# Kernel optimization log

Measured on AMD Instinct MI355X. Metric: run time of the kernel, lower is better.

The kernel has to match this reference:

```python
import jax, jax.numpy as jnp
import numpy as np

D = 256; NH = 8; NL = 4; NP = 4; DFF = 2048; HD = D // NH
SHAPES = [(64, 64), (32, 32), (16, 16), (8, 8)]
B = 2; LEN = sum(h * w for h, w in SHAPES)


def setup_inputs() -> dict:
    key = jax.random.key(0)
    ks = jax.random.split(key, 12)
    def w(k, shape, s=0.02):
        return jax.random.normal(k, shape, jnp.float32) * s
    starts = np.cumsum([0] + [h * w for h, w in SHAPES[:-1]])
    return {
        "src": jax.random.normal(ks[0], (B, LEN, D), jnp.float32),
        "pos": jax.random.normal(ks[1], (B, LEN, D), jnp.float32) * 0.1,
        "spatial_shapes": jnp.array(SHAPES, dtype=jnp.int32),
        "level_start_index": jnp.array(starts, dtype=jnp.int32),
        "w_value": w(ks[2], (D, D)), "b_value": jnp.zeros((D,), jnp.float32),
        "w_off": w(ks[3], (D, NH * NL * NP * 2)), "b_off": w(ks[4], (NH * NL * NP * 2,), 0.1),
        "w_attn": w(ks[5], (D, NH * NL * NP)), "b_attn": jnp.zeros((NH * NL * NP,), jnp.float32),
        "w_out": w(ks[6], (D, D)), "b_out": jnp.zeros((D,), jnp.float32),
        "w1": w(ks[7], (D, DFF)), "b1": jnp.zeros((DFF,), jnp.float32),
        "w2": w(ks[8], (DFF, D)), "b2": jnp.zeros((D,), jnp.float32),
        "g1": jnp.ones((D,), jnp.float32), "be1": jnp.zeros((D,), jnp.float32),
        "g2": jnp.ones((D,), jnp.float32), "be2": jnp.zeros((D,), jnp.float32),
    }


def _layer_norm(x, g, b):
    mu = jnp.mean(x, -1, keepdims=True)
    v = jnp.var(x, -1, keepdims=True)
    return (x - mu) * jax.lax.rsqrt(v + 1e-5) * g + b


def _reference_points(shapes):
    # torch.linspace(0.5, H-0.5, H)/H == (arange(H)+0.5)/H
    refs = []
    for H, W in shapes:
        ry = (jnp.arange(H, dtype=jnp.float32) + 0.5) / H
        rx = (jnp.arange(W, dtype=jnp.float32) + 0.5) / W
        yy, xx = jnp.meshgrid(ry, rx, indexing='ij')
        refs.append(jnp.stack([xx.ravel(), yy.ravel()], -1))
    return jnp.concatenate(refs, 0)  # (Len, 2) as (x, y)


def _ms_deform_sample(value, loc, shapes):
    # value: (B, Len, NH, HD); loc: (B, Lq, NH, NL, NP, 2) normalized [0,1]
    # Replicates torch grid_sample(bilinear, padding='zeros', align_corners=False).
    Bn, Lq = loc.shape[0], loc.shape[1]
    P = loc.shape[4]
    start = 0
    outs = []
    for lvl, (H, W) in enumerate(shapes):
        v = value[:, start:start + H * W].transpose(0, 2, 1, 3)  # (B, NH, HW, HD)
        start += H * W
        l = loc[:, :, :, lvl]                      # (B, Lq, NH, P, 2)
        x = l[..., 0] * W - 0.5
        y = l[..., 1] * H - 0.5
        x0 = jnp.floor(x); y0 = jnp.floor(y)
        dx = x - x0; dy = y - y0
        x0i = x0.astype(jnp.int32); y0i = y0.astype(jnp.int32)
        acc = None
        for xi, yi, wgt in ((x0i, y0i, (1 - dx) * (1 - dy)),
                            (x0i + 1, y0i, dx * (1 - dy)),
                            (x0i, y0i + 1, (1 - dx) * dy),
                            (x0i + 1, y0i + 1, dx * dy)):
            valid = ((xi >= 0) & (xi < W) & (yi >= 0) & (yi < H)).astype(value.dtype)
            idx = jnp.clip(yi, 0, H - 1) * W + jnp.clip(xi, 0, W - 1)  # (B, Lq, NH, P)
            idx = idx.transpose(0, 2, 1, 3).reshape(Bn, NH, Lq * P)
            g = jnp.take_along_axis(v, idx[..., None], axis=2).reshape(Bn, NH, Lq, P, HD)
            w = (wgt * valid).transpose(0, 2, 1, 3)[..., None]  # (B, NH, Lq, P, 1)
            acc = g * w if acc is None else acc + g * w
        outs.append(acc)  # (B, NH, Lq, P, HD)
    return jnp.stack(outs, 3)  # (B, NH, Lq, NL, NP, HD)


def _forward(src, pos, w_value, b_value, w_off, b_off, w_attn, b_attn,
             w_out, b_out, w1, b1, w2, b2, g1, be1, g2, be2, shapes):
    Bn, Lq, _ = src.shape
    q = src + pos  # with_pos_embed
    value = (src @ w_value + b_value).reshape(Bn, Lq, NH, HD)
    off = (q @ w_off + b_off).reshape(Bn, Lq, NH, NL, NP, 2)
    attn = jax.nn.softmax((q @ w_attn + b_attn).reshape(Bn, Lq, NH, NL * NP), -1)
    attn = attn.reshape(Bn, Lq, NH, NL, NP)
    ref = _reference_points(shapes)  # (Len, 2)
    normalizer = jnp.array([[w_, h_] for h_, w_ in shapes], jnp.float32)  # (NL, 2) = (W, H)
    loc = ref[None, :, None, None, None, :] + off / normalizer[None, None, None, :, None, :]
    sampled = _ms_deform_sample(value, loc, shapes)  # (B, NH, Lq, NL, NP, HD)
    out = jnp.einsum('bqhlp,bhqlpd->bqhd', attn, sampled).reshape(Bn, Lq, D)
    out = out @ w_out + b_out
    x = _layer_norm(src + out, g1, be1)           # residual + norm1
    ff = jax.nn.relu(x @ w1 + b1) @ w2 + b2       # FFN (dropout=0)
    return _layer_norm(x + ff, g2, be2)           # residual + norm2


def reference(src, pos, spatial_shapes, level_start_index, w_value, b_value,
              w_off, b_off, w_attn, b_attn, w_out, b_out, w1, b1, w2, b2,
              g1, be1, g2, be2):
    shapes = [tuple(int(v) for v in s) for s in np.asarray(spatial_shapes)]
    return _forward(src, pos, w_value, b_value, w_off, b_off, w_attn, b_attn,
                    w_out, b_out, w1, b1, w2, b2, g1, be1, g2, be2, shapes)
```

## Files before the change

kernel.cpp:

```cpp
#include <hip/hip_runtime.h>
#include <math.h>

#define D 256
#define NH 8
#define NL 4
#define NP 4
#define DFF 2048
#define HD 32
#define BB 2
#define LEN 5440
#define MROWS (BB * LEN)

typedef __attribute__((ext_vector_type(8))) short short8;
typedef __attribute__((ext_vector_type(4))) float f32x4;
typedef unsigned int uint32;

__device__ __forceinline__ unsigned short f2bf(float f) {
    uint32 u = __float_as_uint(f);
    u += 0x7FFF + ((u >> 16) & 1);
    return (unsigned short)(u >> 16);
}
__device__ __forceinline__ float bf2f(unsigned short h) {
    return __uint_as_float(((uint32)h) << 16);
}
__device__ __forceinline__ uint32 pack2(float a, float b) {
    return (uint32)f2bf(a) | ((uint32)f2bf(b) << 16);
}

__device__ __forceinline__ void gl16(const unsigned short* g, unsigned short* l) {
    __builtin_amdgcn_global_load_lds(
        (const __attribute__((address_space(1))) unsigned int*)g,
        (__attribute__((address_space(3))) unsigned int*)l, 16, 0, 0);
}

__device__ __forceinline__ void swz85(int b, int ncols, int& row, int& col) {
    const int gsz = ncols << 3;
    const int full = 10 * gsz;
    if (b < full) {
        const int g = b / gsz, idx = b - g * gsz;
        row = (g << 3) + (idx & 7);
        col = idx >> 3;
    } else {
        const int idx = b - full;
        row = 80 + idx % 5;
        col = idx / 5;
    }
}

__global__ void prep(const float* __restrict__ w_value, const float* __restrict__ w_off,
                     const float* __restrict__ w_attn, const float* __restrict__ w_out,
                     const float* __restrict__ w1, const float* __restrict__ w2,
                     const float* __restrict__ b_value, const float* __restrict__ b_off,
                     const float* __restrict__ b_attn,
                     unsigned short* __restrict__ wqvT, unsigned short* __restrict__ woT,
                     unsigned short* __restrict__ w1T, unsigned short* __restrict__ w2T,
                     float* __restrict__ bqv) {
    const int blk = blockIdx.x;
    if (blk >= 1248) {
        for (int i = threadIdx.x; i < 640; i += 256)
            bqv[i] = (i < 256) ? b_value[i] : (i < 512 ? b_off[i - 256] : b_attn[i - 512]);
        return;
    }
    const float* W; unsigned short* WT; int K, N, tid;
    if (blk < 64)       { W = w_value; WT = wqvT;             K = 256;  N = 256;  tid = blk; }
    else if (blk < 128) { W = w_off;   WT = wqvT + 256 * 256; K = 256;  N = 256;  tid = blk - 64; }
    else if (blk < 160) { W = w_attn;  WT = wqvT + 512 * 256; K = 256;  N = 128;  tid = blk - 128; }
    else if (blk < 224) { W = w_out;   WT = woT;              K = 256;  N = 256;  tid = blk - 160; }
    else if (blk < 736) { W = w1;      WT = w1T;              K = 256;  N = 2048; tid = blk - 224; }
    else                { W = w2;      WT = w2T;              K = 2048; N = 256;  tid = blk - 736; }
    const int ntx = N >> 5;
    const int nb = (tid % ntx) * 32, kb = (tid / ntx) * 32;

    __shared__ float tile[32][33];
    const int tx = threadIdx.x & 31, ty = threadIdx.x >> 5;
#pragma unroll
    for (int i = 0; i < 32; i += 8)
        tile[ty + i][tx] = W[(size_t)(kb + ty + i) * N + nb + tx];
    __syncthreads();
#pragma unroll
    for (int i = 0; i < 32; i += 8)
        WT[(size_t)(nb + ty + i) * K + kb + tx] = f2bf(tile[tx][ty + i]);
}

__global__ __launch_bounds__(256) void ffn1_gemm(
        const unsigned short* __restrict__ A,
        const unsigned short* __restrict__ BT, const float* __restrict__ bias,
        unsigned short* __restrict__ Cv, int N, int K, int lda, int ldb) {
    __shared__ unsigned short Ash[2][128][32];
    __shared__ unsigned short Bsh[2][128][32];

    int rowt, colt;
    swz85(blockIdx.x, N >> 7, rowt, colt);
    const int row0 = rowt * 128, col0 = colt * 128;

    const int t = threadIdx.x;
    const int wave = t >> 6, lane = t & 63;
    const int wr = wave >> 1, wc = wave & 1;
    const int lrow = lane & 15, quad = lane >> 4;
    const int sr = lane >> 2, sc = (lane & 3) * 8;

    const unsigned short* Ab = A + (size_t)row0 * lda;
    const unsigned short* Bb = BT + (size_t)col0 * ldb;

    f32x4 acc[4][4];
#pragma unroll
    for (int i = 0; i < 4; i++)
#pragma unroll
        for (int j = 0; j < 4; j++) acc[i][j] = (f32x4){0.f, 0.f, 0.f, 0.f};

    auto stage = [&](int buf, int kb) {
#pragma unroll
        for (int j = 0; j < 2; j++) {
            const int r = wave * 32 + j * 16;
            gl16(Ab + (size_t)(r + sr) * lda + kb + sc, &Ash[buf][r][0]);
            gl16(Bb + (size_t)(r + sr) * ldb + kb + sc, &Bsh[buf][r][0]);
        }
    };

    stage(0, 0);
    int i = 0;
    for (int kb = 0; kb < K; kb += 32, ++i) {
        __syncthreads();
        if (kb + 32 < K) stage((i + 1) & 1, kb + 32);
        const int cf = i & 1;
        short8 af[4], bfr[4];
#pragma unroll
        for (int mt = 0; mt < 4; mt++)
            af[mt] = *(const short8*)&Ash[cf][wr * 64 + mt * 16 + lrow][quad * 8];
#pragma unroll
        for (int nt = 0; nt < 4; nt++)
            bfr[nt] = *(const short8*)&Bsh[cf][wc * 64 + nt * 16 + lrow][quad * 8];
#pragma unroll
        for (int mt = 0; mt < 4; mt++)
#pragma unroll
            for (int nt = 0; nt < 4; nt++)
                acc[mt][nt] = __builtin_amdgcn_mfma_f32_16x16x32_bf16(
                    af[mt], bfr[nt], acc[mt][nt], 0, 0, 0);
    }

#pragma unroll
    for (int nt = 0; nt < 4; nt++) {
        const int col = col0 + wc * 64 + nt * 16 + lrow;
        const float bv = bias[col];
#pragma unroll
        for (int mt = 0; mt < 4; mt++) {
            f32x4 a = acc[mt][nt];
#pragma unroll
            for (int r = 0; r < 4; r++) {
                const int row = row0 + wr * 64 + mt * 16 + quad * 4 + r;
                Cv[(size_t)row * N + col] = f2bf(fmaxf(a[r] + bv, 0.f));
            }
        }
    }
}

template <int NZ>
__global__ __launch_bounds__(256) void splitk_gemm(
        const unsigned short* __restrict__ A, const unsigned short* __restrict__ BT,
        unsigned short* __restrict__ part, int KC, int lda, int ldb) {
    __shared__ unsigned short Ash[2][128][32];
    __shared__ unsigned short Bsh[2][128][32];

    int rowt, cc;
    swz85(blockIdx.x, 2 * NZ, rowt, cc);
    const int row0 = rowt * 128;
    const int col0 = (cc & 1) * 128;
    const int z = cc >> 1;
    const int koff = z * KC;
    unsigned short* __restrict__ C = part + (size_t)z * MROWS * 256;

    const int t = threadIdx.x;
    const int wave = t >> 6, lane = t & 63;
    const int wr = wave >> 1, wc = wave & 1;
    const int lrow = lane & 15, quad = lane >> 4;
    const int sr = lane >> 2, sc = (lane & 3) * 8;

    const unsigned short* Ab = A + (size_t)row0 * lda + koff;
    const unsigned short* Bb = BT + (size_t)col0 * ldb + koff;

    f32x4 acc[4][4];
#pragma unroll
    for (int i = 0; i < 4; i++)
#pragma unroll
        for (int j = 0; j < 4; j++) acc[i][j] = (f32x4){0.f, 0.f, 0.f, 0.f};

    auto stage = [&](int buf, int kb) {
#pragma unroll
        for (int j = 0; j < 2; j++) {
            const int r = wave * 32 + j * 16;
            gl16(Ab + (size_t)(r + sr) * lda + kb + sc, &Ash[buf][r][0]);
            gl16(Bb + (size_t)(r + sr) * ldb + kb + sc, &Bsh[buf][r][0]);
        }
    };

    stage(0, 0);
    int i = 0;
    for (int kb = 0; kb < KC; kb += 32, ++i) {
        __syncthreads();
        if (kb + 32 < KC) stage((i + 1) & 1, kb + 32);
        const int cf = i & 1;
        short8 af[4], bfr[4];
#pragma unroll
        for (int mt = 0; mt < 4; mt++)
            af[mt] = *(const short8*)&Ash[cf][wr * 64 + mt * 16 + lrow][quad * 8];
#pragma unroll
        for (int nt = 0; nt < 4; nt++)
            bfr[nt] = *(const short8*)&Bsh[cf][wc * 64 + nt * 16 + lrow][quad * 8];
#pragma unroll
        for (int mt = 0; mt < 4; mt++)
#pragma unroll
            for (int nt = 0; nt < 4; nt++)
                acc[mt][nt] = __builtin_amdgcn_mfma_f32_16x16x32_bf16(
                    af[mt], bfr[nt], acc[mt][nt], 0, 0, 0);
    }

#pragma unroll
    for (int nt = 0; nt < 4; nt++) {
        const int col = col0 + wc * 64 + nt * 16 + lrow;
#pragma unroll
        for (int mt = 0; mt < 4; mt++) {
            f32x4 a = acc[mt][nt];
#pragma unroll
            for (int r = 0; r < 4; r++) {
                const int row = row0 + wr * 64 + mt * 16 + quad * 4 + r;
                C[(size_t)row * 256 + col] = f2bf(a[r]);
            }
        }
    }
}

__global__ __launch_bounds__(256) void gemm_ln(
        const unsigned short* __restrict__ A, const unsigned short* __restrict__ BT,
        const float* __restrict__ bias, const float* __restrict__ rsd,
        const float* __restrict__ g, const float* __restrict__ be,
        unsigned short* __restrict__ out16, int K) {
    __shared__ unsigned short Ash[2][32][32];
    __shared__ unsigned short Bsh[2][256][32];
    __shared__ float red1[4][32], red2[4][32];

    const int row0 = blockIdx.x * 32;
    const int t = threadIdx.x;
    const int wave = t >> 6, lane = t & 63;
    const int lrow = lane & 15, quad = lane >> 4;
    const int sr = lane >> 2, sc = (lane & 3) * 8;

    f32x4 acc[2][4];
#pragma unroll
    for (int i = 0; i < 2; i++)
#pragma unroll
        for (int j = 0; j < 4; j++) acc[i][j] = (f32x4){0.f, 0.f, 0.f, 0.f};

    auto stage = [&](int buf, int kb) {
#pragma unroll
        for (int j = 0; j < 4; j++) {
            const int r = wave * 64 + j * 16;
            gl16(BT + (size_t)(r + sr) * K + kb + sc, &Bsh[buf][r][0]);
        }
        if (wave < 2) {
            const int r = wave * 16;
            gl16(A + (size_t)(row0 + r + sr) * K + kb + sc, &Ash[buf][r][0]);
        }
    };

    stage(0, 0);
    int it = 0;
    for (int kb = 0; kb < K; kb += 32, ++it) {
        __syncthreads();
        if (kb + 32 < K) stage((it + 1) & 1, kb + 32);
        const int cf = it & 1;
        short8 af[2], bfr[4];
#pragma unroll
        for (int mt = 0; mt < 2; mt++)
            af[mt] = *(const short8*)&Ash[cf][mt * 16 + lrow][quad * 8];
#pragma unroll
        for (int nt = 0; nt < 4; nt++)
            bfr[nt] = *(const short8*)&Bsh[cf][wave * 64 + nt * 16 + lrow][quad * 8];
#pragma unroll
        for (int mt = 0; mt < 2; mt++)
#pragma unroll
            for (int nt = 0; nt < 4; nt++)
                acc[mt][nt] = __builtin_amdgcn_mfma_f32_16x16x32_bf16(
                    af[mt], bfr[nt], acc[mt][nt], 0, 0, 0);
    }

    float gv[4], bev[4], bv[4];
#pragma unroll
    for (int nt = 0; nt < 4; nt++) {
        const int col = wave * 64 + nt * 16 + lrow;
        bv[nt] = bias[col];
        gv[nt] = g[col];
        bev[nt] = be[col];
    }

    float v[2][4][4];
#pragma unroll
    for (int mt = 0; mt < 2; mt++)
#pragma unroll
        for (int r = 0; r < 4; r++) {
            const int row = row0 + mt * 16 + quad * 4 + r;
#pragma unroll
            for (int nt = 0; nt < 4; nt++) {
                const int col = wave * 64 + nt * 16 + lrow;
                v[mt][nt][r] = acc[mt][nt][r] + bv[nt] + rsd[(size_t)row * 256 + col];
            }
        }

#pragma unroll
    for (int mt = 0; mt < 2; mt++)
#pragma unroll
        for (int r = 0; r < 4; r++) {
            float s1 = v[mt][0][r] + v[mt][1][r] + v[mt][2][r] + v[mt][3][r];
            float s2 = v[mt][0][r] * v[mt][0][r] + v[mt][1][r] * v[mt][1][r] +
                       v[mt][2][r] * v[mt][2][r] + v[mt][3][r] * v[mt][3][r];
#pragma unroll
            for (int o = 1; o < 16; o <<= 1) {
                s1 += __shfl_xor(s1, o, 16);
                s2 += __shfl_xor(s2, o, 16);
            }
            if (lrow == 0) {
                const int rr = mt * 16 + quad * 4 + r;
                red1[wave][rr] = s1;
                red2[wave][rr] = s2;
            }
        }
    __syncthreads();

#pragma unroll
    for (int mt = 0; mt < 2; mt++)
#pragma unroll
        for (int r = 0; r < 4; r++) {
            const int rr = mt * 16 + quad * 4 + r;
            const float su = red1[0][rr] + red1[1][rr] + red1[2][rr] + red1[3][rr];
            const float sq = red2[0][rr] + red2[1][rr] + red2[2][rr] + red2[3][rr];
            const float mean = su * (1.0f / 256.0f);
            const float var = fmaxf(sq * (1.0f / 256.0f) - mean * mean, 0.f);
            const float rstd = rsqrtf(var + 1e-5f);
            const size_t rowoff = (size_t)(row0 + rr) * 256;
#pragma unroll
            for (int nt = 0; nt < 4; nt++) {
                const int col = wave * 64 + nt * 16 + lrow;
                const float o = (v[mt][nt][r] - mean) * rstd * gv[nt] + bev[nt];
                out16[rowoff + col] = f2bf(o);
            }
        }
}

__global__ __launch_bounds__(256) void qv_gemm(
        const float* __restrict__ src, const float* __restrict__ pos,
        const unsigned short* __restrict__ BT, const float* __restrict__ bias,
        unsigned short* __restrict__ val, unsigned short* __restrict__ qout16) {
    __shared__ unsigned short Ash[2][128][40];
    __shared__ unsigned short Bsh[2][128][32];

    int rowt, colt;
    swz85(blockIdx.x, 5, rowt, colt);
    const int row0 = rowt * 128, col0 = colt * 128;
    const bool addp = (col0 >= 256);

    const int t = threadIdx.x;
    const int wave = t >> 6, lane = t & 63;
    const int wr = wave >> 1, wc = wave & 1;
    const int lrow = lane & 15, quad = lane >> 4;
    const int srow = t >> 1;
    const int cb = (t & 1) * 16;
    const int sr = lane >> 2, sc = (lane & 3) * 8;

    const float* ap = src + (size_t)(row0 + srow) * 256 + cb;
    const float* pp = pos + (size_t)(row0 + srow) * 256 + cb;
    const unsigned short* Bb = BT + (size_t)col0 * 256;

    f32x4 acc[4][4];
#pragma unroll
    for (int i = 0; i < 4; i++)
#pragma unroll
        for (int j = 0; j < 4; j++) acc[i][j] = (f32x4){0.f, 0.f, 0.f, 0.f};

    float4 fa[4]; float4 fp[4];
    auto packA = [&](int buf) {
        float4 f0 = fa[0], f1 = fa[1], f2 = fa[2], f3 = fa[3];
        if (addp) {
            f0.x += fp[0].x; f0.y += fp[0].y; f0.z += fp[0].z; f0.w += fp[0].w;
            f1.x += fp[1].x; f1.y += fp[1].y; f1.z += fp[1].z; f1.w += fp[1].w;
            f2.x += fp[2].x; f2.y += fp[2].y; f2.z += fp[2].z; f2.w += fp[2].w;
            f3.x += fp[3].x; f3.y += fp[3].y; f3.z += fp[3].z; f3.w += fp[3].w;
        }
        uint4 u0 = make_uint4(pack2(f0.x, f0.y), pack2(f0.z, f0.w),
                              pack2(f1.x, f1.y), pack2(f1.z, f1.w));
        uint4 u1 = make_uint4(pack2(f2.x, f2.y), pack2(f2.z, f2.w),
                              pack2(f3.x, f3.y), pack2(f3.z, f3.w));
        *(uint4*)&Ash[buf][srow][cb + 0] = u0;
        *(uint4*)&Ash[buf][srow][cb + 8] = u1;
    };
    auto loadA = [&](int kb) {
#pragma unroll
        for (int j = 0; j < 4; j++) fa[j] = *(const float4*)(ap + kb + 4 * j);
        if (addp) {
#pragma unroll
            for (int j = 0; j < 4; j++) fp[j] = *(const float4*)(pp + kb + 4 * j);
        }
    };
    auto stageB = [&](int buf, int kb) {
#pragma unroll
        for (int j = 0; j < 2; j++) {
            const int r = wave * 32 + j * 16;
            gl16(Bb + (size_t)(r + sr) * 256 + kb + sc, &Bsh[buf][r][0]);
        }
    };

    loadA(0);
    packA(0);
    stageB(0, 0);
    loadA(32);

    int i = 0;
    for (int kb = 0; kb < 256; kb += 32, ++i) {
        __syncthreads();
        if (kb + 32 < 256) {
            stageB((i + 1) & 1, kb + 32);
            packA((i + 1) & 1);
            if (kb + 64 < 256) loadA(kb + 64);
        }
        const int cf = i & 1;
        short8 af[4], bfr[4];
#pragma unroll
        for (int mt = 0; mt < 4; mt++)
            af[mt] = *(const short8*)&Ash[cf][wr * 64 + mt * 16 + lrow][quad * 8];
#pragma unroll
        for (int nt = 0; nt < 4; nt++)
            bfr[nt] = *(const short8*)&Bsh[cf][wc * 64 + nt * 16 + lrow][quad * 8];
#pragma unroll
        for (int mt = 0; mt < 4; mt++)
#pragma unroll
            for (int nt = 0; nt < 4; nt++)
                acc[mt][nt] = __builtin_amdgcn_mfma_f32_16x16x32_bf16(
                    af[mt], bfr[nt], acc[mt][nt], 0, 0, 0);
    }

#pragma unroll
    for (int nt = 0; nt < 4; nt++) {
        const int col = col0 + wc * 64 + nt * 16 + lrow;
        const float bv = bias[col];
#pragma unroll
        for (int mt = 0; mt < 4; mt++) {
            f32x4 a = acc[mt][nt];
#pragma unroll
            for (int r = 0; r < 4; r++) {
                const int row = row0 + wr * 64 + mt * 16 + quad * 4 + r;
                float v = a[r] + bv;
                if (col < 256)
                    val[(size_t)row * 256 + col] = f2bf(v);
                else
                    qout16[(size_t)row * 384 + (col - 256)] = f2bf(v);
            }
        }
    }
}

__global__ void sampler(const unsigned short* __restrict__ val,
                        const unsigned short* __restrict__ qout16,
                        unsigned short* __restrict__ out) {
    __shared__ __align__(16) int   sIdx[2][128][4];
    __shared__ __align__(16) float sW[2][128][4];
    const int t = threadIdx.x;
    const int sub = t >> 7;
    const int tt = t & 127;
    const int bq = blockIdx.x * 2 + sub;
    const int b = bq / LEN, q = bq % LEN;

    {
        const int h = tt >> 4, p = tt & 15;
        const int l = p >> 2;

        float refx, refy;
        if (q < 4096) {
            int rq = q >> 6, cq = q & 63;
            refx = (cq + 0.5f) * (1.0f / 64.0f);
            refy = (rq + 0.5f) * (1.0f / 64.0f);
        } else if (q < 5120) {
            int qq = q - 4096;
            int rq = qq >> 5, cq = qq & 31;
            refx = (cq + 0.5f) * (1.0f / 32.0f);
            refy = (rq + 0.5f) * (1.0f / 32.0f);
        } else if (q < 5376) {
            int qq = q - 5120;
            int rq = qq >> 4, cq = qq & 15;
            refx = (cq + 0.5f) * (1.0f / 16.0f);
            refy = (rq + 0.5f) * (1.0f / 16.0f);
        } else {
            int qq = q - 5376;
            int rq = qq >> 3, cq = qq & 7;
            refx = (cq + 0.5f) * (1.0f / 8.0f);
            refy = (rq + 0.5f) * (1.0f / 8.0f);
        }

        float lv = bf2f(qout16[(size_t)bq * 384 + 256 + tt]);
        float mx = lv;
#pragma unroll
        for (int o = 1; o < 16; o <<= 1) mx = fmaxf(mx, __shfl_xor(mx, o, 16));
        float e = expf(lv - mx);
        float s = e;
#pragma unroll
        for (int o = 1; o < 16; o <<= 1) s += __shfl_xor(s, o, 16);
        const float aw = e / s;

        const uint32 opair = *(const uint32*)&qout16[(size_t)bq * 384 + h * 32 + p * 2];
        const float ox = bf2f((unsigned short)opair);
        const float oy = bf2f((unsigned short)(opair >> 16));

        const int LST[4] = {0, 4096, 5120, 5376};
        const int WW = 64 >> l;
        const float rw = 1.0f / (float)WW;

        float x = (refx + ox * rw) * (float)WW - 0.5f;
        float y = (refy + oy * rw) * (float)WW - 0.5f;
        float x0f = floorf(x), y0f = floorf(y);
        float dx = x - x0f, dy = y - y0f;
        int x0 = (int)x0f, y0 = (int)y0f;

        const int base = (b * LEN + LST[l]) * 256 + h * 32;
        int xs[2] = {x0, x0 + 1}, ys[2] = {y0, y0 + 1};
        float wx[2] = {1.f - dx, dx}, wy[2] = {1.f - dy, dy};
        int ic[4]; float wc4[4];
#pragma unroll
        for (int cy = 0; cy < 2; cy++)
#pragma unroll
            for (int cx = 0; cx < 2; cx++) {
                int xi = xs[cx], yi = ys[cy];
                bool vld = (xi >= 0) && (xi < WW) && (yi >= 0) && (yi < WW);
                int xc = min(max(xi, 0), WW - 1);
                int yc = min(max(yi, 0), WW - 1);
                ic[cy * 2 + cx] = base + (yc * WW + xc) * 256;
                wc4[cy * 2 + cx] = vld ? wx[cx] * wy[cy] * aw : 0.f;
            }
        *(int4*)&sIdx[sub][tt][0] = make_int4(ic[0], ic[1], ic[2], ic[3]);
        *(float4*)&sW[sub][tt][0] = make_float4(wc4[0], wc4[1], wc4[2], wc4[3]);
    }
    __syncthreads();

    const int h = tt >> 4, dp = tt & 15;
    const unsigned short* vald = val + 2 * dp;
    float acc0 = 0.f, acc1 = 0.f;
#pragma unroll 4
    for (int p = 0; p < 16; p++) {
        const int r = h * 16 + p;
        int4 iv = *(const int4*)&sIdx[sub][r][0];
        float4 wv = *(const float4*)&sW[sub][r][0];
        uint32 u0 = *(const uint32*)(vald + iv.x);
        uint32 u1 = *(const uint32*)(vald + iv.y);
        uint32 u2 = *(const uint32*)(vald + iv.z);
        uint32 u3 = *(const uint32*)(vald + iv.w);
        acc0 += bf2f((unsigned short)u0) * wv.x + bf2f((unsigned short)u1) * wv.y +
                bf2f((unsigned short)u2) * wv.z + bf2f((unsigned short)u3) * wv.w;
        acc1 += bf2f((unsigned short)(u0 >> 16)) * wv.x + bf2f((unsigned short)(u1 >> 16)) * wv.y +
                bf2f((unsigned short)(u2 >> 16)) * wv.z + bf2f((unsigned short)(u3 >> 16)) * wv.w;
    }
    *(uint32*)&out[(size_t)bq * D + h * HD + 2 * dp] = pack2(acc0, acc1);
}

__global__ void add_ln4(const unsigned short* __restrict__ part16,
                        const float* __restrict__ bias,
                        const unsigned short* __restrict__ rsd16,
                        const float* __restrict__ g, const float* __restrict__ be,
                        float* __restrict__ out) {
    const int wave = threadIdx.x >> 6, lane = threadIdx.x & 63;
    const int row = blockIdx.x * 4 + wave;
    const int c0 = lane * 4;
    const size_t i = (size_t)row * 256 + c0;

    float v[4];
    {
        ushort4 r = *(const ushort4*)&rsd16[i];
        float4 bv = *(const float4*)&bias[c0];
        v[0] = bf2f(r.x) + bv.x; v[1] = bf2f(r.y) + bv.y;
        v[2] = bf2f(r.z) + bv.z; v[3] = bf2f(r.w) + bv.w;
    }
#pragma unroll
    for (int z = 0; z < 4; z++) {
        ushort4 p = *(const ushort4*)&part16[(size_t)z * MROWS * 256 + i];
        v[0] += bf2f(p.x); v[1] += bf2f(p.y); v[2] += bf2f(p.z); v[3] += bf2f(p.w);
    }
    float s1 = v[0] + v[1] + v[2] + v[3];
    float s2 = v[0] * v[0] + v[1] * v[1] + v[2] * v[2] + v[3] * v[3];
#pragma unroll
    for (int o = 32; o > 0; o >>= 1) {
        s1 += __shfl_xor(s1, o, 64);
        s2 += __shfl_xor(s2, o, 64);
    }
    const float mean = s1 * (1.0f / 256.0f);
    const float var = fmaxf(s2 * (1.0f / 256.0f) - mean * mean, 0.f);
    const float rstd = rsqrtf(var + 1e-5f);

    float4 gv = *(const float4*)&g[c0];
    float4 bev = *(const float4*)&be[c0];
    float4 o4;
    o4.x = (v[0] - mean) * rstd * gv.x + bev.x;
    o4.y = (v[1] - mean) * rstd * gv.y + bev.y;
    o4.z = (v[2] - mean) * rstd * gv.z + bev.z;
    o4.w = (v[3] - mean) * rstd * gv.w + bev.w;
    *(float4*)&out[i] = o4;
}

extern "C" void kernel_launch(void* const* d_in, const int* in_sizes, int n_in,
                              void* d_out, int out_size, void* d_ws, size_t ws_size,
                              hipStream_t stream) {
    const float* src     = (const float*)d_in[0];
    const float* pos     = (const float*)d_in[1];
    const float* w_value = (const float*)d_in[4];
    const float* b_value = (const float*)d_in[5];
    const float* w_off   = (const float*)d_in[6];
    const float* b_off   = (const float*)d_in[7];
    const float* w_attn  = (const float*)d_in[8];
    const float* b_attn  = (const float*)d_in[9];
    const float* w_out   = (const float*)d_in[10];
    const float* b_out   = (const float*)d_in[11];
    const float* w1      = (const float*)d_in[12];
    const float* b1      = (const float*)d_in[13];
    const float* w2      = (const float*)d_in[14];
    const float* b2      = (const float*)d_in[15];
    const float* g1      = (const float*)d_in[16];
    const float* be1     = (const float*)d_in[17];
    const float* g2      = (const float*)d_in[18];
    const float* be2     = (const float*)d_in[19];
    float* out = (float*)d_out;

    size_t off = 0;
    auto alloc = [&](size_t bytes) -> char* {
        char* p = (char*)d_ws + off;
        off += (bytes + 255) & ~(size_t)255;
        return p;
    };
    unsigned short* wqvT = (unsigned short*)alloc((size_t)640 * 256 * 2);
    unsigned short* woT  = (unsigned short*)alloc(256 * 256 * 2);
    unsigned short* w1T  = (unsigned short*)alloc((size_t)2048 * 256 * 2);
    unsigned short* w2T  = (unsigned short*)alloc((size_t)256 * 2048 * 2);
    float* bqv           = (float*)alloc(640 * 4);

    unsigned short* qout = (unsigned short*)alloc((size_t)MROWS * 384 * 2);
    unsigned short* val  = (unsigned short*)alloc((size_t)MROWS * 256 * 2);
    unsigned short* attn = (unsigned short*)alloc((size_t)MROWS * 256 * 2);
    unsigned short* hb   = (unsigned short*)alloc((size_t)MROWS * 2048 * 2);
    unsigned short* xb16 = (unsigned short*)alloc((size_t)MROWS * 256 * 2);
    unsigned short* part = (unsigned short*)alloc((size_t)4 * MROWS * 256 * 2);

    prep<<<1249, 256, 0, stream>>>(w_value, w_off, w_attn, w_out, w1, w2,
                                   b_value, b_off, b_attn, wqvT, woT, w1T, w2T, bqv);

    qv_gemm<<<425, 256, 0, stream>>>(src, pos, wqvT, bqv, val, qout);
    sampler<<<MROWS / 2, 256, 0, stream>>>(val, qout, attn);
    gemm_ln<<<340, 256, 0, stream>>>(attn, woT, b_out, src, g1, be1, xb16, 256);

    ffn1_gemm<<<1360, 256, 0, stream>>>(xb16, w1T, b1, hb, 2048, 256, 256, 256);
    splitk_gemm<4><<<680, 256, 0, stream>>>(hb, w2T, part, 512, 2048, 2048);
    add_ln4<<<MROWS / 4, 256, 0, stream>>>(part, b2, xb16, g2, be2, out);
}
```

Baseline: 205.4 us.

## Pre-convert src/pos to bf16, stage GEMM epilogues through LDS, overlap weight prep with sampler

A new prep kernel converts src and src+pos to bf16 once, so the qv GEMM can load its A operand with the same direct global-to-LDS async path it uses for B instead of converting floats in registers. The GEMM epilogues of qv, ffn1 and split-K now write results into a padded LDS bounce buffer and then store 16-byte coalesced rows, replacing scattered 2-byte stores. Transposing the w_out, w1 and w2 weights moves into extra blocks appended to the sampler launch so it can overlap with sampling. The cost is an extra bf16 round trip of the activations through memory, extra barriers in each epilogue, and more shared memory per block.

```diff
diff --git a/kernel.cpp b/kernel.cpp
--- a/kernel.cpp
+++ b/kernel.cpp
@@ -47,47 +47,62 @@
     }
 }
 
-__global__ void prep(const float* __restrict__ w_value, const float* __restrict__ w_off,
-                     const float* __restrict__ w_attn, const float* __restrict__ w_out,
-                     const float* __restrict__ w1, const float* __restrict__ w2,
-                     const float* __restrict__ b_value, const float* __restrict__ b_off,
-                     const float* __restrict__ b_attn,
-                     unsigned short* __restrict__ wqvT, unsigned short* __restrict__ woT,
-                     unsigned short* __restrict__ w1T, unsigned short* __restrict__ w2T,
-                     float* __restrict__ bqv) {
+__global__ void prep_a(const float* __restrict__ w_value, const float* __restrict__ w_off,
+                       const float* __restrict__ w_attn,
+                       const float* __restrict__ b_value, const float* __restrict__ b_off,
+                       const float* __restrict__ b_attn,
+                       const float* __restrict__ src, const float* __restrict__ pos,
+                       unsigned short* __restrict__ wqvT, float* __restrict__ bqv,
+                       unsigned short* __restrict__ s16, unsigned short* __restrict__ q16) {
+    __shared__ float tile[32][33];
     const int blk = blockIdx.x;
-    if (blk >= 1248) {
-        for (int i = threadIdx.x; i < 640; i += 256)
+    const int t = threadIdx.x;
+    if (blk < 160) {
+        const float* W; unsigned short* WT; int N, tid;
+        if (blk < 64)       { W = w_value; WT = wqvT;             N = 256; tid = blk; }
+        else if (blk < 128) { W = w_off;   WT = wqvT + 256 * 256; N = 256; tid = blk - 64; }
+        else                { W = w_attn;  WT = wqvT + 512 * 256; N = 128; tid = blk - 128; }
+        const int K = 256;
+        const int ntx = N >> 5;
+        const int nb = (tid % ntx) * 32, kb = (tid / ntx) * 32;
+        const int tx = t & 31, ty = t >> 5;
+#pragma unroll
+        for (int i = 0; i < 32; i += 8)
+            tile[ty + i][tx] = W[(size_t)(kb + ty + i) * N + nb + tx];
+        __syncthreads();
+#pragma unroll
+        for (int i = 0; i < 32; i += 8)
+            WT[(size_t)(nb + ty + i) * K + kb + tx] = f2bf(tile[tx][ty + i]);
+    } else if (blk == 160) {
+        for (int i = t; i < 640; i += 256)
             bqv[i] = (i < 256) ? b_value[i] : (i < 512 ? b_off[i - 256] : b_attn[i - 512]);
-        return;
-    }
-    const float* W; unsigned short* WT; int K, N, tid;
-    if (blk < 64)       { W = w_value; WT = wqvT;             K = 256;  N = 256;  tid = blk; }
-    else if (blk < 128) { W = w_off;   WT = wqvT + 256 * 256; K = 256;  N = 256;  tid = blk - 64; }
-    else if (blk < 160) { W = w_attn;  WT = wqvT + 512 * 256; K = 256;  N = 128;  tid = blk - 128; }
-    else if (blk < 224) { W = w_out;   WT = woT;              K = 256;  N = 256;  tid = blk - 160; }
-    else if (blk < 736) { W = w1;      WT = w1T;              K = 256;  N = 2048; tid = blk - 224; }
-    else                { W = w2;      WT = w2T;              K = 2048; N = 256;  tid = blk - 736; }
-    const int ntx = N >> 5;
-    const int nb = (tid % ntx) * 32, kb = (tid / ntx) * 32;
-
-    __shared__ float tile[32][33];
-    const int tx = threadIdx.x & 31, ty = threadIdx.x >> 5;
-#pragma unroll
-    for (int i = 0; i < 32; i += 8)
-        tile[ty + i][tx] = W[(size_t)(kb + ty + i) * N + nb + tx];
-    __syncthreads();
-#pragma unroll
-    for (int i = 0; i < 32; i += 8)
-        WT[(size_t)(nb + ty + i) * K + kb + tx] = f2bf(tile[tx][ty + i]);
+    } else {
+        const int tid = blk - 161;
+        const size_t base = (size_t)tid * 4096;
+        const float4* s4 = (const float4*)src;
+        const float4* p4 = (const float4*)pos;
+        ushort4* so = (ushort4*)s16;
+        ushort4* qo = (ushort4*)q16;
+#pragma unroll
+        for (int i = 0; i < 16; i++) {
+            const size_t gidx = base + (size_t)i * 256 + t;
+            float4 a = s4[gidx], p = p4[gidx];
+            ushort4 sv, qv;
+            sv.x = f2bf(a.x); sv.y = f2bf(a.y); sv.z = f2bf(a.z); sv.w = f2bf(a.w);
+            qv.x = f2bf(a.x + p.x); qv.y = f2bf(a.y + p.y);
+            qv.z = f2bf(a.z + p.z); qv.w = f2bf(a.w + p.w);
+            so[gidx] = sv; qo[gidx] = qv;
+        }
+    }
 }
 
 __global__ __launch_bounds__(256) void ffn1_gemm(
         const unsigned short* __restrict__ A,
         const unsigned short* __restrict__ BT, const float* __restrict__ bias,
         unsigned short* __restrict__ Cv, int N, int K, int lda, int ldb) {
-    __shared__ unsigned short Ash[2][128][32];
-    __shared__ unsigned short Bsh[2][128][32];
+    __shared__ unsigned short smraw[17408];
+    auto Ash = (unsigned short (*)[128][32])smraw;
+    auto Bsh = (unsigned short (*)[128][32])(smraw + 8192);
 
     int rowt, colt;
     swz85(blockIdx.x, N >> 7, rowt, colt);
@@ -138,19 +153,26 @@
                     af[mt], bfr[nt], acc[mt][nt], 0, 0, 0);
     }
 
+    __syncthreads();
+    auto bounce = (unsigned short (*)[136])smraw;
 #pragma unroll
     for (int nt = 0; nt < 4; nt++) {
-        const int col = col0 + wc * 64 + nt * 16 + lrow;
-        const float bv = bias[col];
+        const int cl = wc * 64 + nt * 16 + lrow;
+        const float bv = bias[col0 + cl];
 #pragma unroll
         for (int mt = 0; mt < 4; mt++) {
             f32x4 a = acc[mt][nt];
 #pragma unroll
-            for (int r = 0; r < 4; r++) {
-                const int row = row0 + wr * 64 + mt * 16 + quad * 4 + r;
-                Cv[(size_t)row * N + col] = f2bf(fmaxf(a[r] + bv, 0.f));
-            }
-        }
+            for (int r = 0; r < 4; r++)
+                bounce[wr * 64 + mt * 16 + quad * 4 + r][cl] = f2bf(fmaxf(a[r] + bv, 0.f));
+        }
+    }
+    __syncthreads();
+#pragma unroll
+    for (int pass = 0; pass < 8; pass++) {
+        const int rl = pass * 16 + (t >> 4), ch = t & 15;
+        *(uint4*)&Cv[(size_t)(row0 + rl) * N + col0 + ch * 8] =
+            *(const uint4*)&bounce[rl][ch * 8];
     }
 }
 
@@ -158,8 +180,9 @@
 __global__ __launch_bounds__(256) void splitk_gemm(
         const unsigned short* __restrict__ A, const unsigned short* __restrict__ BT,
         unsigned short* __restrict__ part, int KC, int lda, int ldb) {
-    __shared__ unsigned short Ash[2][128][32];
-    __shared__ unsigned short Bsh[2][128][32];
+    __shared__ unsigned short smraw[17408];
+    auto Ash = (unsigned short (*)[128][32])smraw;
+    auto Bsh = (unsigned short (*)[128][32])(smraw + 8192);
 
     int rowt, cc;
     swz85(blockIdx.x, 2 * NZ, rowt, cc);
@@ -214,18 +237,25 @@
                     af[mt], bfr[nt], acc[mt][nt], 0, 0, 0);
     }
 
+    __syncthreads();
+    auto bounce = (unsigned short (*)[136])smraw;
 #pragma unroll
     for (int nt = 0; nt < 4; nt++) {
-        const int col = col0 + wc * 64 + nt * 16 + lrow;
+        const int cl = wc * 64 + nt * 16 + lrow;
 #pragma unroll
         for (int mt = 0; mt < 4; mt++) {
             f32x4 a = acc[mt][nt];
 #pragma unroll
-            for (int r = 0; r < 4; r++) {
-                const int row = row0 + wr * 64 + mt * 16 + quad * 4 + r;
-                C[(size_t)row * 256 + col] = f2bf(a[r]);
-            }
-        }
+            for (int r = 0; r < 4; r++)
+                bounce[wr * 64 + mt * 16 + quad * 4 + r][cl] = f2bf(a[r]);
+        }
+    }
+    __syncthreads();
+#pragma unroll
+    for (int pass = 0; pass < 8; pass++) {
+        const int rl = pass * 16 + (t >> 4), ch = t & 15;
+        *(uint4*)&C[(size_t)(row0 + rl) * 256 + col0 + ch * 8] =
+            *(const uint4*)&bounce[rl][ch * 8];
     }
 }
 
@@ -346,27 +376,24 @@
 }
 
 __global__ __launch_bounds__(256) void qv_gemm(
-        const float* __restrict__ src, const float* __restrict__ pos,
+        const unsigned short* __restrict__ s16, const unsigned short* __restrict__ q16,
         const unsigned short* __restrict__ BT, const float* __restrict__ bias,
         unsigned short* __restrict__ val, unsigned short* __restrict__ qout16) {
-    __shared__ unsigned short Ash[2][128][40];
-    __shared__ unsigned short Bsh[2][128][32];
+    __shared__ unsigned short smraw[17408];
+    auto Ash = (unsigned short (*)[128][32])smraw;
+    auto Bsh = (unsigned short (*)[128][32])(smraw + 8192);
 
     int rowt, colt;
     swz85(blockIdx.x, 5, rowt, colt);
     const int row0 = rowt * 128, col0 = colt * 128;
-    const bool addp = (col0 >= 256);
 
     const int t = threadIdx.x;
     const int wave = t >> 6, lane = t & 63;
     const int wr = wave >> 1, wc = wave & 1;
     const int lrow = lane & 15, quad = lane >> 4;
-    const int srow = t >> 1;
-    const int cb = (t & 1) * 16;
     const int sr = lane >> 2, sc = (lane & 3) * 8;
 
-    const float* ap = src + (size_t)(row0 + srow) * 256 + cb;
-    const float* pp = pos + (size_t)(row0 + srow) * 256 + cb;
+    const unsigned short* Ab = ((col0 >= 256) ? q16 : s16) + (size_t)row0 * 256;
     const unsigned short* Bb = BT + (size_t)col0 * 256;
 
     f32x4 acc[4][4];
@@ -375,51 +402,20 @@
 #pragma unroll
         for (int j = 0; j < 4; j++) acc[i][j] = (f32x4){0.f, 0.f, 0.f, 0.f};
 
-    float4 fa[4]; float4 fp[4];
-    auto packA = [&](int buf) {
-        float4 f0 = fa[0], f1 = fa[1], f2 = fa[2], f3 = fa[3];
-        if (addp) {
-            f0.x += fp[0].x; f0.y += fp[0].y; f0.z += fp[0].z; f0.w += fp[0].w;
-            f1.x += fp[1].x; f1.y += fp[1].y; f1.z += fp[1].z; f1.w += fp[1].w;
-            f2.x += fp[2].x; f2.y += fp[2].y; f2.z += fp[2].z; f2.w += fp[2].w;
-            f3.x += fp[3].x; f3.y += fp[3].y; f3.z += fp[3].z; f3.w += fp[3].w;
-        }
-        uint4 u0 = make_uint4(pack2(f0.x, f0.y), pack2(f0.z, f0.w),
-                              pack2(f1.x, f1.y), pack2(f1.z, f1.w));
-        uint4 u1 = make_uint4(pack2(f2.x, f2.y), pack2(f2.z, f2.w),
-                              pack2(f3.x, f3.y), pack2(f3.z, f3.w));
-        *(uint4*)&Ash[buf][srow][cb + 0] = u0;
-        *(uint4*)&Ash[buf][srow][cb + 8] = u1;
-    };
-    auto loadA = [&](int kb) {
-#pragma unroll
-        for (int j = 0; j < 4; j++) fa[j] = *(const float4*)(ap + kb + 4 * j);
-        if (addp) {
-#pragma unroll
-            for (int j = 0; j < 4; j++) fp[j] = *(const float4*)(pp + kb + 4 * j);
-        }
-    };
-    auto stageB = [&](int buf, int kb) {
+    auto stage = [&](int buf, int kb) {
 #pragma unroll
         for (int j = 0; j < 2; j++) {
             const int r = wave * 32 + j * 16;
+            gl16(Ab + (size_t)(r + sr) * 256 + kb + sc, &Ash[buf][r][0]);
             gl16(Bb + (size_t)(r + sr) * 256 + kb + sc, &Bsh[buf][r][0]);
         }
     };
 
-    loadA(0);
-    packA(0);
-    stageB(0, 0);
-    loadA(32);
-
+    stage(0, 0);
     int i = 0;
     for (int kb = 0; kb < 256; kb += 32, ++i) {
         __syncthreads();
-        if (kb + 32 < 256) {
-            stageB((i + 1) & 1, kb + 32);
-            packA((i + 1) & 1);
-            if (kb + 64 < 256) loadA(kb + 64);
-        }
+        if (kb + 32 < 256) stage((i + 1) & 1, kb + 32);
         const int cf = i & 1;
         short8 af[4], bfr[4];
 #pragma unroll
@@ -436,32 +432,63 @@
                     af[mt], bfr[nt], acc[mt][nt], 0, 0, 0);
     }
 
+    __syncthreads();
+    auto bounce = (unsigned short (*)[136])smraw;
 #pragma unroll
     for (int nt = 0; nt < 4; nt++) {
-        const int col = col0 + wc * 64 + nt * 16 + lrow;
-        const float bv = bias[col];
+        const int cl = wc * 64 + nt * 16 + lrow;
+        const float bv = bias[col0 + cl];
 #pragma unroll
         for (int mt = 0; mt < 4; mt++) {
             f32x4 a = acc[mt][nt];
 #pragma unroll
-            for (int r = 0; r < 4; r++) {
-                const int row = row0 + wr * 64 + mt * 16 + quad * 4 + r;
-                float v = a[r] + bv;
-                if (col < 256)
-                    val[(size_t)row * 256 + col] = f2bf(v);
-                else
-                    qout16[(size_t)row * 384 + (col - 256)] = f2bf(v);
-            }
-        }
+            for (int r = 0; r < 4; r++)
+                bounce[wr * 64 + mt * 16 + quad * 4 + r][cl] = f2bf(a[r] + bv);
+        }
+    }
+    __syncthreads();
+    unsigned short* Cp; int ldc, c0;
+    if (col0 < 256) { Cp = val;    ldc = 256; c0 = col0; }
+    else            { Cp = qout16; ldc = 384; c0 = col0 - 256; }
+#pragma unroll
+    for (int pass = 0; pass < 8; pass++) {
+        const int rl = pass * 16 + (t >> 4), ch = t & 15;
+        *(uint4*)&Cp[(size_t)(row0 + rl) * ldc + c0 + ch * 8] =
+            *(const uint4*)&bounce[rl][ch * 8];
     }
 }
 
 __global__ void sampler(const unsigned short* __restrict__ val,
                         const unsigned short* __restrict__ qout16,
-                        unsigned short* __restrict__ out) {
+                        unsigned short* __restrict__ out,
+                        const float* __restrict__ w_out, const float* __restrict__ w1,
+                        const float* __restrict__ w2,
+                        unsigned short* __restrict__ woT, unsigned short* __restrict__ w1T,
+                        unsigned short* __restrict__ w2T) {
     __shared__ __align__(16) int   sIdx[2][128][4];
     __shared__ __align__(16) float sW[2][128][4];
+    __shared__ float tileT[32][33];
     const int t = threadIdx.x;
+
+    if (blockIdx.x >= MROWS / 2) {
+        const int bk = (int)blockIdx.x - MROWS / 2;
+        const float* W; unsigned short* WT; int K, N, tid;
+        if (bk < 64)       { W = w_out; WT = woT;  K = 256;  N = 256;  tid = bk; }
+        else if (bk < 576) { W = w1;    WT = w1T;  K = 256;  N = 2048; tid = bk - 64; }
+        else               { W = w2;    WT = w2T;  K = 2048; N = 256;  tid = bk - 576; }
+        const int ntx = N >> 5;
+        const int nb = (tid % ntx) * 32, kb = (tid / ntx) * 32;
+        const int tx = t & 31, ty = t >> 5;
+#pragma unroll
+        for (int i = 0; i < 32; i += 8)
+            tileT[ty + i][tx] = W[(size_t)(kb + ty + i) * N + nb + tx];
+        __syncthreads();
+#pragma unroll
+        for (int i = 0; i < 32; i += 8)
+            WT[(size_t)(nb + ty + i) * K + kb + tx] = f2bf(tileT[tx][ty + i]);
+        return;
+    }
+
     const int sub = t >> 7;
     const int tt = t & 127;
     const int bq = blockIdx.x * 2 + sub;
@@ -635,6 +662,8 @@
     unsigned short* w2T  = (unsigned short*)alloc((size_t)256 * 2048 * 2);
     float* bqv           = (float*)alloc(640 * 4);
 
+    unsigned short* s16  = (unsigned short*)alloc((size_t)MROWS * 256 * 2);
+    unsigned short* q16  = (unsigned short*)alloc((size_t)MROWS * 256 * 2);
     unsigned short* qout = (unsigned short*)alloc((size_t)MROWS * 384 * 2);
     unsigned short* val  = (unsigned short*)alloc((size_t)MROWS * 256 * 2);
     unsigned short* attn = (unsigned short*)alloc((size_t)MROWS * 256 * 2);
@@ -642,11 +671,12 @@
     unsigned short* xb16 = (unsigned short*)alloc((size_t)MROWS * 256 * 2);
     unsigned short* part = (unsigned short*)alloc((size_t)4 * MROWS * 256 * 2);
 
-    prep<<<1249, 256, 0, stream>>>(w_value, w_off, w_attn, w_out, w1, w2,
-                                   b_value, b_off, b_attn, wqvT, woT, w1T, w2T, bqv);
-
-    qv_gemm<<<425, 256, 0, stream>>>(src, pos, wqvT, bqv, val, qout);
-    sampler<<<MROWS / 2, 256, 0, stream>>>(val, qout, attn);
+    prep_a<<<331, 256, 0, stream>>>(w_value, w_off, w_attn, b_value, b_off, b_attn,
+                                    src, pos, wqvT, bqv, s16, q16);
+
+    qv_gemm<<<425, 256, 0, stream>>>(s16, q16, wqvT, bqv, val, qout);
+    sampler<<<MROWS / 2 + 1088, 256, 0, stream>>>(val, qout, attn,
+                                                  w_out, w1, w2, woT, w1T, w2T);
     gemm_ln<<<340, 256, 0, stream>>>(attn, woT, b_out, src, g1, be1, xb16, 256);
 
     ffn1_gemm<<<1360, 256, 0, stream>>>(xb16, w1T, b1, hb, 2048, 256, 256, 256);
```

Result: no change. 201.7 us (-1.8%).
